# Optimization experiments

Measured on AMD Instinct MI355X. Metric: run time of the kernel, lower is better.

## Reference

```python
import jax, jax.numpy as jnp
import numpy as np

B, S, E, H = 2, 2048, 1024, 16
D = E // H


def setup_inputs() -> dict:
    key = jax.random.key(0)
    ks = jax.random.split(key, 11)
    def lin(k):
        kw, kb = jax.random.split(k)
        bound = 1.0 / np.sqrt(E)
        W = jax.random.uniform(kw, (E, E), jnp.float32, -bound, bound)
        b = jax.random.uniform(kb, (E,), jnp.float32, -bound, bound)
        return W, b
    Wq, bq = lin(ks[0])
    Wk, bk = lin(ks[1])
    Wv, bv = lin(ks[2])
    Wo, bo = lin(ks[3])
    return {
        "query": jax.random.normal(ks[4], (B, S, E), jnp.float32),
        "key": jax.random.normal(ks[5], (B, S, E), jnp.float32),
        "value": jax.random.normal(ks[6], (B, S, E), jnp.float32),
        "Wq": Wq, "bq": bq, "Wk": Wk, "bk": bk,
        "Wv": Wv, "bv": bv, "Wo": Wo, "bo": bo,
        "is_causal": 1,
    }


def reference(query, key, value, Wq, bq, Wk, bk, Wv, bv, Wo, bo, is_causal):
    scale = D ** -0.5
    def heads(x, W, b):
        # torch Linear: x @ W.T + b, then [B,S,H,D] -> [B,H,S,D]
        y = jnp.einsum('bse,fe->bsf', x, W) + b
        return y.reshape(B, S, H, D).transpose(0, 2, 1, 3)
    q = heads(query, Wq, bq)
    k = heads(key, Wk, bk)
    v = heads(value, Wv, bv)
    scores = jnp.einsum('bhqd,bhkd->bhqk', q, k) * scale  # [B,H,S,S]
    if is_causal:
        mask = jnp.tril(jnp.ones((S, S), dtype=bool))
        scores = jnp.where(mask, scores, -jnp.inf)
    attn = jax.nn.softmax(scores, axis=-1)
    out = jnp.einsum('bhqk,bhkd->bhqd', attn, v)
    out = out.transpose(0, 2, 1, 3).reshape(B, S, E)
    return jnp.einsum('bse,fe->bsf', out, Wo) + bo
```

## Files before the change

kernel.cpp:

```cpp
#include <hip/hip_runtime.h>
#include <cstdint>
#include <cstddef>

typedef unsigned short u16;
typedef unsigned int u32;
typedef __attribute__((ext_vector_type(8))) short bf16x8;
typedef __attribute__((ext_vector_type(4))) float f32x4;
typedef __attribute__((ext_vector_type(16))) float f32x16;
typedef __attribute__((ext_vector_type(4))) u16 u16x4;
typedef __attribute__((ext_vector_type(4))) u32 u32x4;
typedef __attribute__((ext_vector_type(2))) u32 u32x2;

__device__ __forceinline__ u16 f2bf(float f) {
  u32 x = __builtin_bit_cast(u32, f);
  x += 0x7fffu + ((x >> 16) & 1u);
  return (u16)(x >> 16);
}

__device__ __forceinline__ void g2lds16(const u16* g, u16* l) {
  __builtin_amdgcn_global_load_lds(
      (const __attribute__((address_space(1))) u32*)g,
      (__attribute__((address_space(3))) u32*)l, 16, 0, 0);
}

struct CvtArgs { const float* s[7]; u16* d[7]; int n4[7]; };

__global__ __launch_bounds__(256) void cvt_all(CvtArgs a) {
  int y = blockIdx.y;
  const float4* __restrict__ src = (const float4*)a.s[y];
  u16* __restrict__ dst = a.d[y];
  int n4 = a.n4[y];
  for (int i = blockIdx.x * blockDim.x + threadIdx.x; i < n4;
       i += gridDim.x * blockDim.x) {
    float4 v = src[i];
    u16x4 o = { f2bf(v.x), f2bf(v.y), f2bf(v.z), f2bf(v.w) };
    *(u16x4*)(dst + (size_t)i * 4) = o;
  }
}

struct GemmArgs {
  const u16* A[3]; const u16* W[3]; const float* bias[3];
  void* out[3]; float scale[3]; int mode[3];
};

__global__ __launch_bounds__(256) void gemm_fused(GemmArgs ga) {
  __shared__ alignas(16) u16 As[2][128 * 32];
  __shared__ alignas(16) u16 Bs[2][128 * 32];
  const int z = blockIdx.z;
  const u16* __restrict__ A = ga.A[z];
  const u16* __restrict__ W = ga.W[z];
  const int tid = threadIdx.x;
  const int lane = tid & 63;
  const int w = tid >> 6;
  const int lo4 = lane & 15, hi2 = lane >> 4;
  const int l = (int)blockIdx.x + 8 * (int)blockIdx.y;
  const int wl = (l & 7) * 32 + (l >> 3);
  const int m0 = (wl >> 3) * 128;
  const int n0 = (wl & 7) * 128;
  const int wr = w >> 1, wc = w & 1;

  f32x4 acc[4][4] = {};

  auto stage = [&](int kt, int buf) {
    const int k0 = kt * 32;
#pragma unroll
    for (int i = 0; i < 2; ++i) {
      int c = (i * 4 + w) * 64 + lane;
      int r = c >> 2;
      int q = (c & 3) ^ ((r >> 1) & 3);
      g2lds16(A + (size_t)(m0 + r) * 1024 + k0 + q * 8, As[buf] + (i * 4 + w) * 512);
      g2lds16(W + (size_t)(n0 + r) * 1024 + k0 + q * 8, Bs[buf] + (i * 4 + w) * 512);
    }
  };

  stage(0, 0);
  stage(1, 1);
  for (int kt = 0; kt < 32; ++kt) {
    const int cur = kt & 1;
    asm volatile("s_waitcnt vmcnt(4)" ::: "memory");
    __builtin_amdgcn_s_barrier();
    bf16x8 af[4], bfr[4];
#pragma unroll
    for (int i = 0; i < 4; ++i) {
      int r = wr * 64 + i * 16 + lo4;
      int q = hi2 ^ ((r >> 1) & 3);
      af[i] = *(const bf16x8*)(As[cur] + r * 32 + q * 8);
    }
#pragma unroll
    for (int j = 0; j < 4; ++j) {
      int r = wc * 64 + j * 16 + lo4;
      int q = hi2 ^ ((r >> 1) & 3);
      bfr[j] = *(const bf16x8*)(Bs[cur] + r * 32 + q * 8);
    }
#pragma unroll
    for (int i = 0; i < 4; ++i)
#pragma unroll
      for (int j = 0; j < 4; ++j)
        acc[i][j] = __builtin_amdgcn_mfma_f32_16x16x32_bf16(af[i], bfr[j], acc[i][j], 0, 0, 0);
    __builtin_amdgcn_s_barrier();
    stage(kt + 2 < 32 ? kt + 2 : kt, cur);
  }
  asm volatile("s_waitcnt vmcnt(0)" ::: "memory");

  const float* __restrict__ bias = ga.bias[z];
  const float cs = ga.scale[z];
  const int mode = ga.mode[z];
#pragma unroll
  for (int j = 0; j < 4; ++j) {
    int n = n0 + wc * 64 + j * 16 + lo4;
    float bv = bias[n];
#pragma unroll
    for (int i = 0; i < 4; ++i) {
#pragma unroll
      for (int rg = 0; rg < 4; ++rg) {
        int m = m0 + wr * 64 + i * 16 + hi2 * 4 + rg;
        float v = (acc[i][j][rg] + bv) * cs;
        if (mode == 2) {
          ((float*)ga.out[z])[(size_t)m * 1024 + n] = v;
        } else {
          int b = m >> 11, s = m & 2047, h = n >> 6, d = n & 63;
          size_t addr = (mode == 0)
            ? ((size_t)(b * 16 + h) * 2048 + s) * 64 + d
            : ((size_t)(b * 16 + h) * 64 + d) * 2048 + s;
          ((u16*)ga.out[z])[addr] = f2bf(v);
        }
      }
    }
  }
}

__global__ __launch_bounds__(256, 2) void attn_kernel(
    const u16* __restrict__ Q, const u16* __restrict__ K,
    const u16* __restrict__ Vt, u16* __restrict__ Out,
    const int* __restrict__ causal_p) {
  __shared__ alignas(16) u16 Ks[2][2][64 * 64];
  __shared__ alignas(16) u16 Vs[2][2][64 * 64];
  const int tid = threadIdx.x, lane = tid & 63, w = tid >> 6;
  const int wg = w >> 1, wv = w & 1;
  const int ql = lane & 31, hi = lane >> 5;
  const int bh = blockIdx.y;
  const int qt = (bh < 16) ? (int)blockIdx.x : 15 - (int)blockIdx.x;
  const int causal = *causal_p;
  const u16* Qb = Q + (size_t)bh * 2048 * 64;
  const u16* Kb = K + (size_t)bh * 2048 * 64;
  const u16* Vb = Vt + (size_t)bh * 64 * 2048;

  const int qA = qt * 128 + wv * 64 + ql;
  const int qB = qA + 32;

  bf16x8 qfA[4], qfB[4];
#pragma unroll
  for (int dsl = 0; dsl < 4; ++dsl) {
    qfA[dsl] = *(const bf16x8*)(Qb + (size_t)qA * 64 + dsl * 16 + hi * 8);
    qfB[dsl] = *(const bf16x8*)(Qb + (size_t)qB * 64 + dsl * 16 + hi * 8);
  }

  auto stageKV = [&](int jt, int buf) {
#pragma unroll
    for (int i = 0; i < 4; ++i) {
      int c = i * 128 + wv * 64 + lane;
      int r = c >> 3;
      int q = (c & 7) ^ (r & 7);
      g2lds16(Kb + (size_t)(jt * 64 + r) * 64 + q * 8, Ks[wg][buf] + (i * 128 + wv * 64) * 8);
      g2lds16(Vb + (size_t)r * 2048 + jt * 64 + q * 8, Vs[wg][buf] + (i * 128 + wv * 64) * 8);
    }
  };

  const int nt_w = causal ? (2 * qt + wv + 1) : 32;
  const int U = causal ? (qt + 1) : 16;

  stageKV(wg, 0);
  stageKV(wg + 2, 1);
  float mA = -1e30f, lA = 0.f, mB = -1e30f, lB = 0.f;
  f32x16 oA0 = {}, oA1 = {}, oB0 = {}, oB1 = {};

  auto online_sm = [&](f32x16& s0, f32x16& s1, float& m_r, float& l_r,
                       f32x16& o0, f32x16& o1) {
    float pm = fmaxf(s0[0], s1[0]);
#pragma unroll
    for (int rg = 1; rg < 16; ++rg) pm = fmaxf(pm, fmaxf(s0[rg], s1[rg]));
    pm = fmaxf(pm, __shfl_xor(pm, 32));
    if (!__all(pm <= m_r + 8.f)) {
      float mn = fmaxf(m_r, pm);
      float corr = exp2f(m_r - mn);
      m_r = mn; l_r *= corr;
#pragma unroll
      for (int rg = 0; rg < 16; ++rg) { o0[rg] *= corr; o1[rg] *= corr; }
    }
    float sum = 0.f;
#pragma unroll
    for (int rg = 0; rg < 16; ++rg) { s0[rg] = exp2f(s0[rg] - m_r); sum += s0[rg]; }
#pragma unroll
    for (int rg = 0; rg < 16; ++rg) { s1[rg] = exp2f(s1[rg] - m_r); sum += s1[rg]; }
    sum += __shfl_xor(sum, 32);
    l_r += sum;
  };

  for (int u = 0; u < U; ++u) {
    const int jt = 2 * u + wg;
    const int cur = u & 1;
    asm volatile("s_waitcnt vmcnt(8)" ::: "memory");
    __builtin_amdgcn_s_barrier();

    if (jt < nt_w) {
      f32x16 sA0 = {}, sA1 = {}, sB0 = {}, sB1 = {};
#pragma unroll
      for (int dsl = 0; dsl < 4; ++dsl) {
        int cc = dsl * 2 + hi;
        bf16x8 k0 = *(const bf16x8*)(Ks[wg][cur] + ql * 64 + ((cc ^ (ql & 7)) * 8));
        bf16x8 k1 = *(const bf16x8*)(Ks[wg][cur] + (32 + ql) * 64 + ((cc ^ (ql & 7)) * 8));
        sA0 = __builtin_amdgcn_mfma_f32_32x32x16_bf16(k0, qfA[dsl], sA0, 0, 0, 0);
        sB0 = __builtin_amdgcn_mfma_f32_32x32x16_bf16(k0, qfB[dsl], sB0, 0, 0, 0);
        sA1 = __builtin_amdgcn_mfma_f32_32x32x16_bf16(k1, qfA[dsl], sA1, 0, 0, 0);
        sB1 = __builtin_amdgcn_mfma_f32_32x32x16_bf16(k1, qfB[dsl], sB1, 0, 0, 0);
      }

      if (causal && jt == nt_w - 1) {
#pragma unroll
        for (int rg = 0; rg < 16; ++rg) {
          int kof = jt * 64 + 8 * (rg >> 2) + (rg & 3) + 4 * hi;
          sA0[rg] = (kof > qA) ? -1e30f : sA0[rg];
          sA1[rg] = (kof + 32 > qA) ? -1e30f : sA1[rg];
          sB0[rg] = (kof > qB) ? -1e30f : sB0[rg];
          sB1[rg] = (kof + 32 > qB) ? -1e30f : sB1[rg];
        }
      }

      online_sm(sA0, sA1, mA, lA, oA0, oA1);
      online_sm(sB0, sB1, mB, lB, oB0, oB1);

#pragma unroll
      for (int s = 0; s < 4; ++s) {
        const f32x16& pA = (s >= 2) ? sA1 : sA0;
        const f32x16& pB = (s >= 2) ? sB1 : sB0;
        const int base = 8 * (s & 1);
        u32 a0, a1, b0, b1, c0, c1, d0_, d1;
        asm("v_cvt_pk_bf16_f32 %0, %1, %2" : "=v"(a0) : "v"(pA[base + 0]), "v"(pA[base + 1]));
        asm("v_cvt_pk_bf16_f32 %0, %1, %2" : "=v"(a1) : "v"(pA[base + 2]), "v"(pA[base + 3]));
        asm("v_cvt_pk_bf16_f32 %0, %1, %2" : "=v"(b0) : "v"(pA[base + 4]), "v"(pA[base + 5]));
        asm("v_cvt_pk_bf16_f32 %0, %1, %2" : "=v"(b1) : "v"(pA[base + 6]), "v"(pA[base + 7]));
        asm volatile("v_permlane32_swap_b32 %0, %1" : "+v"(a0), "+v"(b0));
        asm volatile("v_permlane32_swap_b32 %0, %1" : "+v"(a1), "+v"(b1));
        asm("v_cvt_pk_bf16_f32 %0, %1, %2" : "=v"(c0) : "v"(pB[base + 0]), "v"(pB[base + 1]));
        asm("v_cvt_pk_bf16_f32 %0, %1, %2" : "=v"(c1) : "v"(pB[base + 2]), "v"(pB[base + 3]));
        asm("v_cvt_pk_bf16_f32 %0, %1, %2" : "=v"(d0_) : "v"(pB[base + 4]), "v"(pB[base + 5]));
        asm("v_cvt_pk_bf16_f32 %0, %1, %2" : "=v"(d1) : "v"(pB[base + 6]), "v"(pB[base + 7]));
        asm volatile("v_permlane32_swap_b32 %0, %1" : "+v"(c0), "+v"(d0_));
        asm volatile("v_permlane32_swap_b32 %0, %1" : "+v"(c1), "+v"(d1));
        u32x4 pwA = {a0, a1, b0, b1};
        u32x4 pwB = {c0, c1, d0_, d1};
        bf16x8 pfA = __builtin_bit_cast(bf16x8, pwA);
        bf16x8 pfB = __builtin_bit_cast(bf16x8, pwB);
#pragma unroll
        for (int df = 0; df < 2; ++df) {
          int rr = df * 32 + ql;
          bf16x8 vf = *(const bf16x8*)(Vs[wg][cur] + rr * 64 + (((s * 2 + hi) ^ (rr & 7)) * 8));
          if (df) {
            oA1 = __builtin_amdgcn_mfma_f32_32x32x16_bf16(vf, pfA, oA1, 0, 0, 0);
            oB1 = __builtin_amdgcn_mfma_f32_32x32x16_bf16(vf, pfB, oB1, 0, 0, 0);
          } else {
            oA0 = __builtin_amdgcn_mfma_f32_32x32x16_bf16(vf, pfA, oA0, 0, 0, 0);
            oB0 = __builtin_amdgcn_mfma_f32_32x32x16_bf16(vf, pfB, oB0, 0, 0, 0);
          }
        }
      }
    }
    __builtin_amdgcn_s_barrier();
    stageKV(u + 2 < U ? jt + 4 : jt, cur);
  }
  asm volatile("s_waitcnt vmcnt(0)" ::: "memory");
  __syncthreads();

  float* Od = (float*)&Ks[0][0][0];
  float* ml = (float*)&Vs[0][0][0];
  const int li = wv * 64 + lane;
  if (wg == 1) {
#pragma unroll
    for (int rg = 0; rg < 16; ++rg) {
      Od[((li * 2 + 0) * 2 + 0) * 16 + rg] = oA0[rg];
      Od[((li * 2 + 0) * 2 + 1) * 16 + rg] = oA1[rg];
      Od[((li * 2 + 1) * 2 + 0) * 16 + rg] = oB0[rg];
      Od[((li * 2 + 1) * 2 + 1) * 16 + rg] = oB1[rg];
    }
    ml[li * 4 + 0] = mA; ml[li * 4 + 1] = lA;
    ml[li * 4 + 2] = mB; ml[li * 4 + 3] = lB;
  }
  __syncthreads();
  if (wg == 0) {
    const int batch = bh >> 4, h = bh & 15;
#pragma unroll
    for (int sub = 0; sub < 2; ++sub) {
      float m_r = sub ? mB : mA;
      float l_r = sub ? lB : lA;
      float m_b = ml[li * 4 + sub * 2 + 0];
      float l_b = ml[li * 4 + sub * 2 + 1];
      float mn = fmaxf(m_r, m_b);
      float ca = exp2f(m_r - mn), cb = exp2f(m_b - mn);
      float rl = 1.f / (l_r * ca + l_b * cb);
      int qrow = sub ? qB : qA;
      u16* orow = Out + ((size_t)(batch * 2048 + qrow)) * 1024 + h * 64;
#pragma unroll
      for (int df = 0; df < 2; ++df) {
        const f32x16& oo = sub ? (df ? oB1 : oB0) : (df ? oA1 : oA0);
        const float* Op = &Od[((li * 2 + sub) * 2 + df) * 16];
#pragma unroll
        for (int b2 = 0; b2 < 4; ++b2) {
          u32 w0, w1;
          float v0 = (oo[4 * b2 + 0] * ca + Op[4 * b2 + 0] * cb) * rl;
          float v1 = (oo[4 * b2 + 1] * ca + Op[4 * b2 + 1] * cb) * rl;
          float v2 = (oo[4 * b2 + 2] * ca + Op[4 * b2 + 2] * cb) * rl;
          float v3 = (oo[4 * b2 + 3] * ca + Op[4 * b2 + 3] * cb) * rl;
          asm("v_cvt_pk_bf16_f32 %0, %1, %2" : "=v"(w0) : "v"(v0), "v"(v1));
          asm("v_cvt_pk_bf16_f32 %0, %1, %2" : "=v"(w1) : "v"(v2), "v"(v3));
          int d0 = df * 32 + b2 * 8 + hi * 4;
          u32x2 pr = {w0, w1};
          *(u32x2*)(orow + d0) = pr;
        }
      }
    }
  }
}

extern "C" void kernel_launch(void* const* d_in, const int* in_sizes, int n_in,
                              void* d_out, int out_size, void* d_ws, size_t ws_size,
                              hipStream_t stream) {
  (void)in_sizes; (void)n_in; (void)out_size; (void)ws_size;
  const float* query = (const float*)d_in[0];
  const float* key   = (const float*)d_in[1];
  const float* value = (const float*)d_in[2];
  const float* Wq = (const float*)d_in[3];
  const float* bq = (const float*)d_in[4];
  const float* Wk = (const float*)d_in[5];
  const float* bk = (const float*)d_in[6];
  const float* Wv = (const float*)d_in[7];
  const float* bv = (const float*)d_in[8];
  const float* Wo = (const float*)d_in[9];
  const float* bo = (const float*)d_in[10];
  const int* is_causal = (const int*)d_in[11];

  u16* wsp = (u16*)d_ws;
  u16* xq  = wsp;
  u16* xk  = xq  + (4u << 20);
  u16* xv  = xk  + (4u << 20);
  u16* wq  = xv  + (4u << 20);
  u16* wk  = wq  + (1u << 20);
  u16* wv  = wk  + (1u << 20);
  u16* wo  = wv  + (1u << 20);
  u16* Qb  = wo  + (1u << 20);
  u16* Kb  = Qb  + (4u << 20);
  u16* Vtb = Kb  + (4u << 20);
  u16* attn= Vtb + (4u << 20);

  CvtArgs ca;
  ca.s[0] = query; ca.d[0] = xq; ca.n4[0] = 1 << 20;
  ca.s[1] = key;   ca.d[1] = xk; ca.n4[1] = 1 << 20;
  ca.s[2] = value; ca.d[2] = xv; ca.n4[2] = 1 << 20;
  ca.s[3] = Wq; ca.d[3] = wq; ca.n4[3] = 1 << 18;
  ca.s[4] = Wk; ca.d[4] = wk; ca.n4[4] = 1 << 18;
  ca.s[5] = Wv; ca.d[5] = wv; ca.n4[5] = 1 << 18;
  ca.s[6] = Wo; ca.d[6] = wo; ca.n4[6] = 1 << 18;
  cvt_all<<<dim3(512, 7), 256, 0, stream>>>(ca);

  const float LOG2E = 1.4426950408889634f;
  GemmArgs g1;
  g1.A[0] = xq; g1.W[0] = wq; g1.bias[0] = bq; g1.out[0] = Qb;
  g1.scale[0] = 0.125f * LOG2E; g1.mode[0] = 0;
  g1.A[1] = xk; g1.W[1] = wk; g1.bias[1] = bk; g1.out[1] = Kb;
  g1.scale[1] = 1.f; g1.mode[1] = 0;
  g1.A[2] = xv; g1.W[2] = wv; g1.bias[2] = bv; g1.out[2] = Vtb;
  g1.scale[2] = 1.f; g1.mode[2] = 1;
  gemm_fused<<<dim3(8, 32, 3), 256, 0, stream>>>(g1);

  attn_kernel<<<dim3(16, 32), 256, 0, stream>>>(Qb, Kb, Vtb, attn, is_causal);

  GemmArgs g2;
  for (int i = 0; i < 3; ++i) {
    g2.A[i] = attn; g2.W[i] = wo; g2.bias[i] = bo; g2.out[i] = d_out;
    g2.scale[i] = 1.f; g2.mode[i] = 2;
  }
  gemm_fused<<<dim3(8, 32, 1), 256, 0, stream>>>(g2);
}
```

Measured before the change: 136.0 us.

## Widen attention blocks to four KV-split wave groups and pair causal tiles

The attention kernel now launches 512-thread blocks with four wave groups. The groups split the key/value tiles four ways instead of two, and their partial softmax states are merged serially through LDS. Each block processes two query tiles (slot and 15-slot) in sequence, which balances causal work per block, and the block-to-head mapping is permuted across the grid. This should raise parallelism per query tile and even out the load, at the cost of more LDS use, extra barriers and a serial three-step merge.

```diff
diff --git a/kernel.cpp b/kernel.cpp
--- a/kernel.cpp
+++ b/kernel.cpp
@@ -129,50 +129,43 @@
   }
 }
 
-__global__ __launch_bounds__(256, 2) void attn_kernel(
+__global__ __launch_bounds__(512, 2) void attn_kernel(
     const u16* __restrict__ Q, const u16* __restrict__ K,
     const u16* __restrict__ Vt, u16* __restrict__ Out,
     const int* __restrict__ causal_p) {
-  __shared__ alignas(16) u16 Ks[2][2][64 * 64];
-  __shared__ alignas(16) u16 Vs[2][2][64 * 64];
+  __shared__ alignas(16) u16 Ks[4][2][64 * 64];
+  __shared__ alignas(16) u16 Vs[4][2][64 * 64];
+  __shared__ float ml2[512];
   const int tid = threadIdx.x, lane = tid & 63, w = tid >> 6;
   const int wg = w >> 1, wv = w & 1;
   const int ql = lane & 31, hi = lane >> 5;
-  const int bh = blockIdx.y;
-  const int qt = (bh < 16) ? (int)blockIdx.x : 15 - (int)blockIdx.x;
+  const int L = (int)blockIdx.x + 8 * (int)blockIdx.y;
+  const int bh = (L & 7) * 4 + ((int)blockIdx.y >> 3);
+  const int slot = (int)blockIdx.y & 7;
   const int causal = *causal_p;
   const u16* Qb = Q + (size_t)bh * 2048 * 64;
   const u16* Kb = K + (size_t)bh * 2048 * 64;
   const u16* Vb = Vt + (size_t)bh * 64 * 2048;
-
-  const int qA = qt * 128 + wv * 64 + ql;
-  const int qB = qA + 32;
-
-  bf16x8 qfA[4], qfB[4];
-#pragma unroll
-  for (int dsl = 0; dsl < 4; ++dsl) {
-    qfA[dsl] = *(const bf16x8*)(Qb + (size_t)qA * 64 + dsl * 16 + hi * 8);
-    qfB[dsl] = *(const bf16x8*)(Qb + (size_t)qB * 64 + dsl * 16 + hi * 8);
-  }
+  const int batch = bh >> 4, h = bh & 15;
 
   auto stageKV = [&](int jt, int buf) {
 #pragma unroll
-    for (int i = 0; i < 4; ++i) {
+    for (int i = 0; i < 2; ++i) {
       int c = i * 128 + wv * 64 + lane;
       int r = c >> 3;
       int q = (c & 7) ^ (r & 7);
       g2lds16(Kb + (size_t)(jt * 64 + r) * 64 + q * 8, Ks[wg][buf] + (i * 128 + wv * 64) * 8);
       g2lds16(Vb + (size_t)r * 2048 + jt * 64 + q * 8, Vs[wg][buf] + (i * 128 + wv * 64) * 8);
     }
+#pragma unroll
+    for (int i = 2; i < 4; ++i) {
+      int c = i * 128 + wv * 64 + lane;
+      int r = c >> 3;
+      int q = (c & 7) ^ (r & 7);
+      g2lds16(Kb + (size_t)(jt * 64 + r) * 64 + q * 8, Ks[wg][buf] + (i * 128 + wv * 64) * 8);
+      g2lds16(Vb + (size_t)r * 2048 + jt * 64 + q * 8, Vs[wg][buf] + (i * 128 + wv * 64) * 8);
+    }
   };
-
-  const int nt_w = causal ? (2 * qt + wv + 1) : 32;
-  const int U = causal ? (qt + 1) : 16;
-
-  stageKV(wg, 0);
-  stageKV(wg + 2, 1);
-  float mA = -1e30f, lA = 0.f, mB = -1e30f, lB = 0.f;
-  f32x16 oA0 = {}, oA1 = {}, oB0 = {}, oB1 = {};
 
   auto online_sm = [&](f32x16& s0, f32x16& s1, float& m_r, float& l_r,
                        f32x16& o0, f32x16& o1) {
@@ -196,128 +189,173 @@
     l_r += sum;
   };
 
-  for (int u = 0; u < U; ++u) {
-    const int jt = 2 * u + wg;
-    const int cur = u & 1;
-    asm volatile("s_waitcnt vmcnt(8)" ::: "memory");
-    __builtin_amdgcn_s_barrier();
-
-    if (jt < nt_w) {
-      f32x16 sA0 = {}, sA1 = {}, sB0 = {}, sB1 = {};
-#pragma unroll
-      for (int dsl = 0; dsl < 4; ++dsl) {
-        int cc = dsl * 2 + hi;
-        bf16x8 k0 = *(const bf16x8*)(Ks[wg][cur] + ql * 64 + ((cc ^ (ql & 7)) * 8));
-        bf16x8 k1 = *(const bf16x8*)(Ks[wg][cur] + (32 + ql) * 64 + ((cc ^ (ql & 7)) * 8));
-        sA0 = __builtin_amdgcn_mfma_f32_32x32x16_bf16(k0, qfA[dsl], sA0, 0, 0, 0);
-        sB0 = __builtin_amdgcn_mfma_f32_32x32x16_bf16(k0, qfB[dsl], sB0, 0, 0, 0);
-        sA1 = __builtin_amdgcn_mfma_f32_32x32x16_bf16(k1, qfA[dsl], sA1, 0, 0, 0);
-        sB1 = __builtin_amdgcn_mfma_f32_32x32x16_bf16(k1, qfB[dsl], sB1, 0, 0, 0);
-      }
-
-      if (causal && jt == nt_w - 1) {
-#pragma unroll
-        for (int rg = 0; rg < 16; ++rg) {
-          int kof = jt * 64 + 8 * (rg >> 2) + (rg & 3) + 4 * hi;
-          sA0[rg] = (kof > qA) ? -1e30f : sA0[rg];
-          sA1[rg] = (kof + 32 > qA) ? -1e30f : sA1[rg];
-          sB0[rg] = (kof > qB) ? -1e30f : sB0[rg];
-          sB1[rg] = (kof + 32 > qB) ? -1e30f : sB1[rg];
+  float* Od = (float*)&Ks[0][0][0];
+  const int li = wv * 64 + lane;
+
+  for (int seg = 0; seg < 2; ++seg) {
+    const int qt = seg ? 15 - slot : slot;
+    const int qA = qt * 128 + wv * 64 + ql;
+    const int qB = qA + 32;
+
+    bf16x8 qfA[4], qfB[4];
+#pragma unroll
+    for (int dsl = 0; dsl < 4; ++dsl) {
+      qfA[dsl] = *(const bf16x8*)(Qb + (size_t)qA * 64 + dsl * 16 + hi * 8);
+      qfB[dsl] = *(const bf16x8*)(Qb + (size_t)qB * 64 + dsl * 16 + hi * 8);
+    }
+
+    const int nt_w = causal ? (2 * qt + wv + 1) : 32;
+    const int U = causal ? ((2 * qt + 5) >> 2) : 8;
+
+    stageKV(wg, 0);
+    stageKV(wg + 4, 1);
+
+    float mA = -1e30f, lA = 0.f, mB = -1e30f, lB = 0.f;
+    f32x16 oA0 = {}, oA1 = {}, oB0 = {}, oB1 = {};
+
+    for (int u = 0; u < U; ++u) {
+      const int jt = 4 * u + wg;
+      const int cur = u & 1;
+      asm volatile("s_waitcnt vmcnt(8)" ::: "memory");
+      __builtin_amdgcn_s_barrier();
+
+      if (jt < nt_w) {
+        f32x16 sA0 = {}, sA1 = {}, sB0 = {}, sB1 = {};
+#pragma unroll
+        for (int dsl = 0; dsl < 4; ++dsl) {
+          int cc = dsl * 2 + hi;
+          bf16x8 k0 = *(const bf16x8*)(Ks[wg][cur] + ql * 64 + ((cc ^ (ql & 7)) * 8));
+          bf16x8 k1 = *(const bf16x8*)(Ks[wg][cur] + (32 + ql) * 64 + ((cc ^ (ql & 7)) * 8));
+          sA0 = __builtin_amdgcn_mfma_f32_32x32x16_bf16(k0, qfA[dsl], sA0, 0, 0, 0);
+          sB0 = __builtin_amdgcn_mfma_f32_32x32x16_bf16(k0, qfB[dsl], sB0, 0, 0, 0);
+          sA1 = __builtin_amdgcn_mfma_f32_32x32x16_bf16(k1, qfA[dsl], sA1, 0, 0, 0);
+          sB1 = __builtin_amdgcn_mfma_f32_32x32x16_bf16(k1, qfB[dsl], sB1, 0, 0, 0);
         }
-      }
-
-      online_sm(sA0, sA1, mA, lA, oA0, oA1);
-      online_sm(sB0, sB1, mB, lB, oB0, oB1);
-
-#pragma unroll
-      for (int s = 0; s < 4; ++s) {
-        const f32x16& pA = (s >= 2) ? sA1 : sA0;
-        const f32x16& pB = (s >= 2) ? sB1 : sB0;
-        const int base = 8 * (s & 1);
-        u32 a0, a1, b0, b1, c0, c1, d0_, d1;
-        asm("v_cvt_pk_bf16_f32 %0, %1, %2" : "=v"(a0) : "v"(pA[base + 0]), "v"(pA[base + 1]));
-        asm("v_cvt_pk_bf16_f32 %0, %1, %2" : "=v"(a1) : "v"(pA[base + 2]), "v"(pA[base + 3]));
-        asm("v_cvt_pk_bf16_f32 %0, %1, %2" : "=v"(b0) : "v"(pA[base + 4]), "v"(pA[base + 5]));
-        asm("v_cvt_pk_bf16_f32 %0, %1, %2" : "=v"(b1) : "v"(pA[base + 6]), "v"(pA[base + 7]));
-        asm volatile("v_permlane32_swap_b32 %0, %1" : "+v"(a0), "+v"(b0));
-        asm volatile("v_permlane32_swap_b32 %0, %1" : "+v"(a1), "+v"(b1));
-        asm("v_cvt_pk_bf16_f32 %0, %1, %2" : "=v"(c0) : "v"(pB[base + 0]), "v"(pB[base + 1]));
-        asm("v_cvt_pk_bf16_f32 %0, %1, %2" : "=v"(c1) : "v"(pB[base + 2]), "v"(pB[base + 3]));
-        asm("v_cvt_pk_bf16_f32 %0, %1, %2" : "=v"(d0_) : "v"(pB[base + 4]), "v"(pB[base + 5]));
-        asm("v_cvt_pk_bf16_f32 %0, %1, %2" : "=v"(d1) : "v"(pB[base + 6]), "v"(pB[base + 7]));
-        asm volatile("v_permlane32_swap_b32 %0, %1" : "+v"(c0), "+v"(d0_));
-        asm volatile("v_permlane32_swap_b32 %0, %1" : "+v"(c1), "+v"(d1));
-        u32x4 pwA = {a0, a1, b0, b1};
-        u32x4 pwB = {c0, c1, d0_, d1};
-        bf16x8 pfA = __builtin_bit_cast(bf16x8, pwA);
-        bf16x8 pfB = __builtin_bit_cast(bf16x8, pwB);
-#pragma unroll
-        for (int df = 0; df < 2; ++df) {
-          int rr = df * 32 + ql;
-          bf16x8 vf = *(const bf16x8*)(Vs[wg][cur] + rr * 64 + (((s * 2 + hi) ^ (rr & 7)) * 8));
-          if (df) {
-            oA1 = __builtin_amdgcn_mfma_f32_32x32x16_bf16(vf, pfA, oA1, 0, 0, 0);
-            oB1 = __builtin_amdgcn_mfma_f32_32x32x16_bf16(vf, pfB, oB1, 0, 0, 0);
-          } else {
-            oA0 = __builtin_amdgcn_mfma_f32_32x32x16_bf16(vf, pfA, oA0, 0, 0, 0);
-            oB0 = __builtin_amdgcn_mfma_f32_32x32x16_bf16(vf, pfB, oB0, 0, 0, 0);
+
+        if (causal && jt == nt_w - 1) {
+#pragma unroll
+          for (int rg = 0; rg < 16; ++rg) {
+            int kof = jt * 64 + 8 * (rg >> 2) + (rg & 3) + 4 * hi;
+            sA0[rg] = (kof > qA) ? -1e30f : sA0[rg];
+            sA1[rg] = (kof + 32 > qA) ? -1e30f : sA1[rg];
+            sB0[rg] = (kof > qB) ? -1e30f : sB0[rg];
+            sB1[rg] = (kof + 32 > qB) ? -1e30f : sB1[rg];
           }
         }
-      }
-    }
-    __builtin_amdgcn_s_barrier();
-    stageKV(u + 2 < U ? jt + 4 : jt, cur);
-  }
-  asm volatile("s_waitcnt vmcnt(0)" ::: "memory");
-  __syncthreads();
-
-  float* Od = (float*)&Ks[0][0][0];
-  float* ml = (float*)&Vs[0][0][0];
-  const int li = wv * 64 + lane;
-  if (wg == 1) {
-#pragma unroll
-    for (int rg = 0; rg < 16; ++rg) {
-      Od[((li * 2 + 0) * 2 + 0) * 16 + rg] = oA0[rg];
-      Od[((li * 2 + 0) * 2 + 1) * 16 + rg] = oA1[rg];
-      Od[((li * 2 + 1) * 2 + 0) * 16 + rg] = oB0[rg];
-      Od[((li * 2 + 1) * 2 + 1) * 16 + rg] = oB1[rg];
-    }
-    ml[li * 4 + 0] = mA; ml[li * 4 + 1] = lA;
-    ml[li * 4 + 2] = mB; ml[li * 4 + 3] = lB;
-  }
-  __syncthreads();
-  if (wg == 0) {
-    const int batch = bh >> 4, h = bh & 15;
-#pragma unroll
-    for (int sub = 0; sub < 2; ++sub) {
-      float m_r = sub ? mB : mA;
-      float l_r = sub ? lB : lA;
-      float m_b = ml[li * 4 + sub * 2 + 0];
-      float l_b = ml[li * 4 + sub * 2 + 1];
-      float mn = fmaxf(m_r, m_b);
-      float ca = exp2f(m_r - mn), cb = exp2f(m_b - mn);
-      float rl = 1.f / (l_r * ca + l_b * cb);
-      int qrow = sub ? qB : qA;
-      u16* orow = Out + ((size_t)(batch * 2048 + qrow)) * 1024 + h * 64;
-#pragma unroll
-      for (int df = 0; df < 2; ++df) {
-        const f32x16& oo = sub ? (df ? oB1 : oB0) : (df ? oA1 : oA0);
-        const float* Op = &Od[((li * 2 + sub) * 2 + df) * 16];
-#pragma unroll
-        for (int b2 = 0; b2 < 4; ++b2) {
-          u32 w0, w1;
-          float v0 = (oo[4 * b2 + 0] * ca + Op[4 * b2 + 0] * cb) * rl;
-          float v1 = (oo[4 * b2 + 1] * ca + Op[4 * b2 + 1] * cb) * rl;
-          float v2 = (oo[4 * b2 + 2] * ca + Op[4 * b2 + 2] * cb) * rl;
-          float v3 = (oo[4 * b2 + 3] * ca + Op[4 * b2 + 3] * cb) * rl;
-          asm("v_cvt_pk_bf16_f32 %0, %1, %2" : "=v"(w0) : "v"(v0), "v"(v1));
-          asm("v_cvt_pk_bf16_f32 %0, %1, %2" : "=v"(w1) : "v"(v2), "v"(v3));
-          int d0 = df * 32 + b2 * 8 + hi * 4;
-          u32x2 pr = {w0, w1};
-          *(u32x2*)(orow + d0) = pr;
+
+        online_sm(sA0, sA1, mA, lA, oA0, oA1);
+        online_sm(sB0, sB1, mB, lB, oB0, oB1);
+
+#pragma unroll
+        for (int s = 0; s < 4; ++s) {
+          const f32x16& pA = (s >= 2) ? sA1 : sA0;
+          const f32x16& pB = (s >= 2) ? sB1 : sB0;
+          const int base = 8 * (s & 1);
+          u32 a0, a1, b0, b1, c0, c1, d0_, d1;
+          asm("v_cvt_pk_bf16_f32 %0, %1, %2" : "=v"(a0) : "v"(pA[base + 0]), "v"(pA[base + 1]));
+          asm("v_cvt_pk_bf16_f32 %0, %1, %2" : "=v"(a1) : "v"(pA[base + 2]), "v"(pA[base + 3]));
+          asm("v_cvt_pk_bf16_f32 %0, %1, %2" : "=v"(b0) : "v"(pA[base + 4]), "v"(pA[base + 5]));
+          asm("v_cvt_pk_bf16_f32 %0, %1, %2" : "=v"(b1) : "v"(pA[base + 6]), "v"(pA[base + 7]));
+          asm volatile("v_permlane32_swap_b32 %0, %1" : "+v"(a0), "+v"(b0));
+          asm volatile("v_permlane32_swap_b32 %0, %1" : "+v"(a1), "+v"(b1));
+          asm("v_cvt_pk_bf16_f32 %0, %1, %2" : "=v"(c0) : "v"(pB[base + 0]), "v"(pB[base + 1]));
+          asm("v_cvt_pk_bf16_f32 %0, %1, %2" : "=v"(c1) : "v"(pB[base + 2]), "v"(pB[base + 3]));
+          asm("v_cvt_pk_bf16_f32 %0, %1, %2" : "=v"(d0_) : "v"(pB[base + 4]), "v"(pB[base + 5]));
+          asm("v_cvt_pk_bf16_f32 %0, %1, %2" : "=v"(d1) : "v"(pB[base + 6]), "v"(pB[base + 7]));
+          asm volatile("v_permlane32_swap_b32 %0, %1" : "+v"(c0), "+v"(d0_));
+          asm volatile("v_permlane32_swap_b32 %0, %1" : "+v"(c1), "+v"(d1));
+          u32x4 pwA = {a0, a1, b0, b1};
+          u32x4 pwB = {c0, c1, d0_, d1};
+          bf16x8 pfA = __builtin_bit_cast(bf16x8, pwA);
+          bf16x8 pfB = __builtin_bit_cast(bf16x8, pwB);
+#pragma unroll
+          for (int df = 0; df < 2; ++df) {
+            int rr = df * 32 + ql;
+            bf16x8 vf = *(const bf16x8*)(Vs[wg][cur] + rr * 64 + (((s * 2 + hi) ^ (rr & 7)) * 8));
+            if (df) {
+              oA1 = __builtin_amdgcn_mfma_f32_32x32x16_bf16(vf, pfA, oA1, 0, 0, 0);
+              oB1 = __builtin_amdgcn_mfma_f32_32x32x16_bf16(vf, pfB, oB1, 0, 0, 0);
+            } else {
+              oA0 = __builtin_amdgcn_mfma_f32_32x32x16_bf16(vf, pfA, oA0, 0, 0, 0);
+              oB0 = __builtin_amdgcn_mfma_f32_32x32x16_bf16(vf, pfB, oB0, 0, 0, 0);
+            }
+          }
         }
       }
-    }
+      __builtin_amdgcn_s_barrier();
+      stageKV(u + 2 < U ? 4 * (u + 2) + wg : jt, cur);
+    }
+    asm volatile("s_waitcnt vmcnt(0)" ::: "memory");
+    __syncthreads();
+
+    auto store_partial = [&]() {
+#pragma unroll
+      for (int rg = 0; rg < 16; ++rg) {
+        Od[li * 64 + rg]      = oA0[rg];
+        Od[li * 64 + 16 + rg] = oA1[rg];
+        Od[li * 64 + 32 + rg] = oB0[rg];
+        Od[li * 64 + 48 + rg] = oB1[rg];
+      }
+      ml2[li * 4 + 0] = mA; ml2[li * 4 + 1] = lA;
+      ml2[li * 4 + 2] = mB; ml2[li * 4 + 3] = lB;
+    };
+    auto merge_partial = [&]() {
+      float m_b = ml2[li * 4 + 0], l_b = ml2[li * 4 + 1];
+      float mn = fmaxf(mA, m_b);
+      float ca = exp2f(mA - mn), cb = exp2f(m_b - mn);
+      mA = mn; lA = lA * ca + l_b * cb;
+#pragma unroll
+      for (int rg = 0; rg < 16; ++rg) {
+        oA0[rg] = oA0[rg] * ca + Od[li * 64 + rg] * cb;
+        oA1[rg] = oA1[rg] * ca + Od[li * 64 + 16 + rg] * cb;
+      }
+      m_b = ml2[li * 4 + 2]; l_b = ml2[li * 4 + 3];
+      mn = fmaxf(mB, m_b);
+      ca = exp2f(mB - mn); cb = exp2f(m_b - mn);
+      mB = mn; lB = lB * ca + l_b * cb;
+#pragma unroll
+      for (int rg = 0; rg < 16; ++rg) {
+        oB0[rg] = oB0[rg] * ca + Od[li * 64 + 32 + rg] * cb;
+        oB1[rg] = oB1[rg] * ca + Od[li * 64 + 48 + rg] * cb;
+      }
+    };
+
+    if (wg == 1) store_partial();
+    __syncthreads();
+    if (wg == 0) merge_partial();
+    __syncthreads();
+    if (wg == 2) store_partial();
+    __syncthreads();
+    if (wg == 0) merge_partial();
+    __syncthreads();
+    if (wg == 3) store_partial();
+    __syncthreads();
+
+    if (wg == 0) {
+      merge_partial();
+#pragma unroll
+      for (int sub = 0; sub < 2; ++sub) {
+        float rl = 1.f / (sub ? lB : lA);
+        int qrow = sub ? qB : qA;
+        u16* orow = Out + ((size_t)(batch * 2048 + qrow)) * 1024 + h * 64;
+#pragma unroll
+        for (int df = 0; df < 2; ++df) {
+          const f32x16& oo = sub ? (df ? oB1 : oB0) : (df ? oA1 : oA0);
+#pragma unroll
+          for (int b2 = 0; b2 < 4; ++b2) {
+            u32 w0, w1;
+            float v0 = oo[4 * b2 + 0] * rl, v1 = oo[4 * b2 + 1] * rl;
+            float v2 = oo[4 * b2 + 2] * rl, v3 = oo[4 * b2 + 3] * rl;
+            asm("v_cvt_pk_bf16_f32 %0, %1, %2" : "=v"(w0) : "v"(v0), "v"(v1));
+            asm("v_cvt_pk_bf16_f32 %0, %1, %2" : "=v"(w1) : "v"(v2), "v"(v3));
+            int d0 = df * 32 + b2 * 8 + hi * 4;
+            u32x2 pr = {w0, w1};
+            *(u32x2*)(orow + d0) = pr;
+          }
+        }
+      }
+    }
+    __syncthreads();
   }
 }
 
@@ -371,7 +409,7 @@
   g1.scale[2] = 1.f; g1.mode[2] = 1;
   gemm_fused<<<dim3(8, 32, 3), 256, 0, stream>>>(g1);
 
-  attn_kernel<<<dim3(16, 32), 256, 0, stream>>>(Qb, Kb, Vtb, attn, is_causal);
+  attn_kernel<<<dim3(8, 32), 512, 0, stream>>>(Qb, Kb, Vtb, attn, is_causal);
 
   GemmArgs g2;
   for (int i = 0; i < 3; ++i) {
```

Measured after the change: 139.7 us. +2.7%, slower.
